# Kernel optimization log

Measured on AMD Instinct MI355X. Metric: run time of the kernel, lower is better.

## Reference

```python
import jax, jax.numpy as jnp
import numpy as np

IN_FEATURES = 512
OUT_FEATURES = 512
N_HEADS = 512
BATCH = 1024
N_REGIONS = 128


def setup_inputs() -> dict:
    key = jax.random.key(0)
    k1, k2, k3, k4 = jax.random.split(key, 4)
    # Match torch's uniform(-stdv, stdv) init scale (stdv = 1/sqrt(last dim))
    stdv_w = 1.0 / np.sqrt(OUT_FEATURES)
    stdv_b = 1.0 / np.sqrt(OUT_FEATURES)
    inputs = {
        "input": jax.random.normal(k1, (IN_FEATURES, BATCH), dtype=jnp.float32),
        "regions_oi": jax.random.randint(k2, (N_REGIONS,), 0, N_HEADS),
        "weight_table": jax.random.uniform(
            k3, (N_HEADS, IN_FEATURES, OUT_FEATURES), dtype=jnp.float32,
            minval=-stdv_w, maxval=stdv_w),
        "bias_table": jax.random.uniform(
            k4, (N_HEADS, OUT_FEATURES), dtype=jnp.float32,
            minval=-stdv_b, maxval=stdv_b),
    }
    return inputs


def reference(input, regions_oi, weight_table, bias_table):
    # Gather per-region weights/biases (EmbeddingTensor lookup)
    w = weight_table[regions_oi]   # (C, A, D) = (n_regions, in_features, out_features)
    b = bias_table[regions_oi]     # (C, D)
    # torch.einsum('ab,cad->cbd', input, w) + b[:, None, :]
    out = jnp.einsum('ab,cad->cbd', input, w) + b[:, None, :]  # (C, B, D)
    return out
```

## Files before the change

kernel.cpp:

```cpp
#include <hip/hip_runtime.h>
#include <stdint.h>

#define A_DIM 512
#define B_DIM 1024
#define D_DIM 512
#define NKT   16

typedef __bf16 bf16x8 __attribute__((ext_vector_type(8)));
typedef float f32x4 __attribute__((ext_vector_type(4)));
typedef unsigned u32x2 __attribute__((ext_vector_type(2)));

typedef __attribute__((address_space(1))) void gvoid_t;
typedef __attribute__((address_space(3))) void svoid_t;

#define WAITV8() asm volatile("s_waitcnt vmcnt(8)" ::: "memory")
#define WAITV0() asm volatile("s_waitcnt vmcnt(0)" ::: "memory")
#define LGKM0()  asm volatile("s_waitcnt lgkmcnt(0)" ::: "memory")
#define FENCE()  asm volatile("" ::: "memory")
#define BARRIER() do { FENCE(); __builtin_amdgcn_s_barrier(); FENCE(); } while (0)

__device__ __forceinline__ unsigned short f2bf(float f) {
  union { float f; unsigned u; } x; x.f = f;
  unsigned r = x.u + 0x7fffu + ((x.u >> 16) & 1u);
  return (unsigned short)(r >> 16);
}

__device__ __forceinline__ unsigned pk2(float lo, float hi) {
  unsigned r;
  asm("v_cvt_pk_bf16_f32 %0, %1, %2" : "=v"(r) : "v"(lo), "v"(hi));
  return r;
}

__device__ __forceinline__ void gload16(const void* g, void* l) {
  __builtin_amdgcn_global_load_lds((gvoid_t*)g, (svoid_t*)l, 16, 0, 0);
}

__global__ __launch_bounds__(256) void transpose_cvt(
    const float* __restrict__ src, unsigned short* __restrict__ dst,
    int M, int N) {
  __shared__ float T[64][65];
  const int t = threadIdx.x;
  const int m0 = blockIdx.y * 64, n0 = blockIdx.x * 64;

#pragma unroll
  for (int p = 0; p < 4; ++p) {
    const int mr = (t >> 4) + p * 16;
    const int n4 = (t & 15) * 4;
    const float4 v = *(const float4*)(src + (size_t)(m0 + mr) * N + n0 + n4);
    T[n4 + 0][mr] = v.x;
    T[n4 + 1][mr] = v.y;
    T[n4 + 2][mr] = v.z;
    T[n4 + 3][mr] = v.w;
  }
  __syncthreads();

#pragma unroll
  for (int p = 0; p < 2; ++p) {
    const int nr = (t >> 3) + p * 32;
    const int m8 = (t & 7) * 8;
    alignas(16) unsigned short tmp[8];
#pragma unroll
    for (int j = 0; j < 8; ++j) tmp[j] = f2bf(T[nr][m8 + j]);
    *(uint4*)(dst + (size_t)(n0 + nr) * M + m0 + m8) = *(const uint4*)tmp;
  }
}

__global__ __launch_bounds__(256, 2) void mlgemm_fused(
    const unsigned short* __restrict__ Xt, const float* __restrict__ wtab,
    const float* __restrict__ bias_table, const int* __restrict__ regions,
    float* __restrict__ out) {
  __shared__ union SM {
    struct {
      alignas(16) unsigned short As[3][256][32];
      alignas(16) unsigned Bsu[2][16][130];
    } k;
    alignas(16) float slab[4][32 * 68];
  } sm;

  const int bid = blockIdx.x;
  const int xcd = bid & 7, q = bid >> 3;
  const int c   = (q >> 4) * 8 + xcd;
  const int t16 = q & 15;
  const int b0     = (t16 & 3) * 256;
  const int d0blk  = (t16 >> 2) * 128;

  const int t = threadIdx.x;
  const int w = t >> 6, l = t & 63;
  const int lr = l & 15, lg = l >> 4;
  const int wm = w >> 1, wn = w & 1;
  const int h = regions[c];

  const unsigned short* Xbase = Xt + (size_t)b0 * A_DIM;
  const float* Wbase = wtab + (size_t)h * A_DIM * D_DIM + d0blk;

  f32x4 acc[8][4] = {};

  const int a_src_chunk = (l & 3) ^ ((l >> 3) & 3);
  const int a_lrow = l >> 2;
  const int kp_base = (w & 1) * 4 + ((l >> 3) & 3);
  const int bd0 = 4 * (l & 7) + 32 * (l >> 5) + 64 * (w >> 1);

  f32x4 bregE[4], bregO[4];

  auto issueA = [&](int T) {
    const int buf = T % 3;
    const int koff = T * 32 + a_src_chunk * 8;
#pragma unroll
    for (int i = 0; i < 4; ++i) {
      const int row0 = w * 64 + i * 16;
      gload16(Xbase + (size_t)(row0 + a_lrow) * A_DIM + koff, &sm.k.As[buf][row0][0]);
    }
  };
  auto ldB = [&](int T, f32x4 (&breg)[4]) {
#pragma unroll
    for (int r = 0; r < 2; ++r) {
      const int kp = r * 8 + kp_base;
      const float* p = Wbase + (size_t)(T * 32 + kp * 2) * D_DIM + bd0;
      breg[r * 2 + 0] = *(const f32x4*)p;
      breg[r * 2 + 1] = *(const f32x4*)(p + D_DIM);
    }
  };
  auto writeB = [&](int T, f32x4 (&breg)[4]) {
#pragma unroll
    for (int r = 0; r < 2; ++r) {
      const int kp = r * 8 + kp_base;
      unsigned pk[4];
#pragma unroll
      for (int i = 0; i < 4; ++i)
        pk[i] = pk2(breg[r * 2][i], breg[r * 2 + 1][i]);
      unsigned* dst = &sm.k.Bsu[T & 1][kp][bd0];
      *(u32x2*)(dst + 0) = u32x2{pk[0], pk[1]};
      *(u32x2*)(dst + 2) = u32x2{pk[2], pk[3]};
    }
  };

  auto mfmaStep = [&](int T) {
    const int abuf = T % 3, bbuf = T & 1;
    bf16x8 av[8], bv[4];
#pragma unroll
    for (int m = 0; m < 8; ++m) {
      const int row = wm * 128 + m * 16 + lr;
      av[m] = *(const bf16x8*)&sm.k.As[abuf][row][(lg ^ ((lr >> 1) & 3)) * 8];
    }
#pragma unroll
    for (int n = 0; n < 4; ++n) {
      const int d = wn * 64 + n * 16 + lr;
      union { unsigned u[4]; bf16x8 v; } ub;
#pragma unroll
      for (int i = 0; i < 4; ++i) ub.u[i] = sm.k.Bsu[bbuf][4 * lg + i][d];
      bv[n] = ub.v;
    }
    __builtin_amdgcn_s_setprio(1);
#pragma unroll
    for (int m = 0; m < 8; ++m)
#pragma unroll
      for (int n = 0; n < 4; ++n)
        acc[m][n] = __builtin_amdgcn_mfma_f32_16x16x32_bf16(av[m], bv[n], acc[m][n], 0, 0, 0);
    __builtin_amdgcn_s_setprio(0);
  };

  float bs[4];
#pragma unroll
  for (int n = 0; n < 4; ++n)
    bs[n] = bias_table[(size_t)h * D_DIM + d0blk + wn * 64 + n * 16 + lr];

  issueA(0); ldB(0, bregE);
  issueA(1); ldB(1, bregO);

#pragma unroll 1
  for (int T = 0; T < NKT - 2; T += 2) {
    WAITV8();
    writeB(T, bregE);
    LGKM0(); BARRIER();
    issueA(T + 2); ldB(T + 2, bregE); FENCE();
    mfmaStep(T);

    WAITV8();
    writeB(T + 1, bregO);
    LGKM0(); BARRIER();
    issueA(T + 3); ldB(T + 3, bregO); FENCE();
    mfmaStep(T + 1);
  }
  WAITV8();
  writeB(NKT - 2, bregE);
  LGKM0(); BARRIER();
  mfmaStep(NKT - 2);
  WAITV0();
  writeB(NKT - 1, bregO);
  LGKM0(); BARRIER();
  mfmaStep(NKT - 1);

  __syncthreads();

  float* ob = out + (size_t)c * B_DIM * D_DIM;
  const int orow_base = b0 + wm * 128;
  const int ocol_base = d0blk + wn * 64;
#pragma unroll
  for (int g = 0; g < 4; ++g) {
#pragma unroll
    for (int m2 = 0; m2 < 2; ++m2)
#pragma unroll
      for (int j = 0; j < 4; ++j) {
        const int row = m2 * 16 + lg * 4 + j;
#pragma unroll
        for (int n = 0; n < 4; ++n)
          sm.slab[w][row * 68 + n * 16 + lr] = acc[g * 2 + m2][n][j] + bs[n];
      }
    __syncthreads();
#pragma unroll
    for (int r = 0; r < 8; ++r) {
      const int chunk = r * 64 + l;
      const int row = chunk >> 4, seg = chunk & 15;
      const f32x4 v = *(const f32x4*)&sm.slab[w][row * 68 + seg * 4];
      __builtin_nontemporal_store(
          v, (f32x4*)(ob + (size_t)(orow_base + g * 32 + row) * D_DIM +
                      ocol_base + seg * 4));
    }
    __syncthreads();
  }
}

__global__ __launch_bounds__(256) void naive_ml(
    const float* __restrict__ in, const int* __restrict__ regions,
    const float* __restrict__ wt, const float* __restrict__ bias,
    float* __restrict__ out) {
  const int d = blockIdx.x * 256 + threadIdx.x;
  const int b = blockIdx.y;
  const int cz = blockIdx.z;
  const int hh = regions[cz];
  const float* W = wt + (size_t)hh * A_DIM * D_DIM + d;
  float acc = bias[(size_t)hh * D_DIM + d];
  for (int a = 0; a < A_DIM; ++a) acc += in[(size_t)a * B_DIM + b] * W[(size_t)a * D_DIM];
  out[(size_t)cz * B_DIM * D_DIM + (size_t)b * D_DIM + d] = acc;
}

extern "C" void kernel_launch(void* const* d_in, const int* in_sizes, int n_in,
                              void* d_out, int out_size, void* d_ws, size_t ws_size,
                              hipStream_t stream) {
  const float* input = (const float*)d_in[0];
  const int* regions = (const int*)d_in[1];
  const float* wtab  = (const float*)d_in[2];
  const float* btab  = (const float*)d_in[3];
  float* out = (float*)d_out;
  const int C = in_sizes[1];

  const size_t xt_bytes = (size_t)B_DIM * A_DIM * 2;

  if (ws_size < xt_bytes) {
    naive_ml<<<dim3(D_DIM / 256, B_DIM, C), 256, 0, stream>>>(input, regions, wtab, btab, out);
    return;
  }

  unsigned short* Xt = (unsigned short*)d_ws;

  transpose_cvt<<<dim3(B_DIM / 64, A_DIM / 64), 256, 0, stream>>>(
      input, Xt, A_DIM, B_DIM);
  mlgemm_fused<<<dim3((B_DIM / 256) * (D_DIM / 128) * C), 256, 0, stream>>>(
      Xt, wtab, btab, regions, out);
}
```

Before: 110.4 us.

## Repack B tile in LDS as k-quad rows for 8-byte fragment reads

Changes how the fp32 weight tile is loaded and staged in LDS. Each wave now loads contiguous 8-byte pairs across the full 128-wide d range for four consecutive k rows, packs them into bf16 quads, and writes one 16-byte store per half. The MFMA B fragment then comes from two 8-byte LDS reads instead of four scalar reads. The vmcnt wait threshold rises to 12 to match the larger number of outstanding global loads per stage. The aim is fewer LDS instructions and cheaper B fragment assembly, at the cost of narrower global loads and possible new bank conflicts.

```diff
diff --git a/kernel.cpp b/kernel.cpp
--- a/kernel.cpp
+++ b/kernel.cpp
@@ -8,15 +8,16 @@
 
 typedef __bf16 bf16x8 __attribute__((ext_vector_type(8)));
 typedef float f32x4 __attribute__((ext_vector_type(4)));
+typedef float f32x2 __attribute__((ext_vector_type(2)));
 typedef unsigned u32x2 __attribute__((ext_vector_type(2)));
 
 typedef __attribute__((address_space(1))) void gvoid_t;
 typedef __attribute__((address_space(3))) void svoid_t;
 
-#define WAITV8() asm volatile("s_waitcnt vmcnt(8)" ::: "memory")
-#define WAITV0() asm volatile("s_waitcnt vmcnt(0)" ::: "memory")
-#define LGKM0()  asm volatile("s_waitcnt lgkmcnt(0)" ::: "memory")
-#define FENCE()  asm volatile("" ::: "memory")
+#define WAITV12() asm volatile("s_waitcnt vmcnt(12)" ::: "memory")
+#define WAITV0()  asm volatile("s_waitcnt vmcnt(0)" ::: "memory")
+#define LGKM0()   asm volatile("s_waitcnt lgkmcnt(0)" ::: "memory")
+#define FENCE()   asm volatile("" ::: "memory")
 #define BARRIER() do { FENCE(); __builtin_amdgcn_s_barrier(); FENCE(); } while (0)
 
 __device__ __forceinline__ unsigned short f2bf(float f) {
@@ -72,7 +73,7 @@
   __shared__ union SM {
     struct {
       alignas(16) unsigned short As[3][256][32];
-      alignas(16) unsigned Bsu[2][16][130];
+      alignas(16) unsigned Bsu[2][8][264];
     } k;
     alignas(16) float slab[4][32 * 68];
   } sm;
@@ -97,10 +98,8 @@
 
   const int a_src_chunk = (l & 3) ^ ((l >> 3) & 3);
   const int a_lrow = l >> 2;
-  const int kp_base = (w & 1) * 4 + ((l >> 3) & 3);
-  const int bd0 = 4 * (l & 7) + 32 * (l >> 5) + 64 * (w >> 1);
-
-  f32x4 bregE[4], bregO[4];
+
+  f32x2 bregE[8], bregO[8];
 
   auto issueA = [&](int T) {
     const int buf = T % 3;
@@ -111,26 +110,28 @@
       gload16(Xbase + (size_t)(row0 + a_lrow) * A_DIM + koff, &sm.k.As[buf][row0][0]);
     }
   };
-  auto ldB = [&](int T, f32x4 (&breg)[4]) {
-#pragma unroll
-    for (int r = 0; r < 2; ++r) {
-      const int kp = r * 8 + kp_base;
-      const float* p = Wbase + (size_t)(T * 32 + kp * 2) * D_DIM + bd0;
-      breg[r * 2 + 0] = *(const f32x4*)p;
-      breg[r * 2 + 1] = *(const f32x4*)(p + D_DIM);
-    }
-  };
-  auto writeB = [&](int T, f32x4 (&breg)[4]) {
-#pragma unroll
-    for (int r = 0; r < 2; ++r) {
-      const int kp = r * 8 + kp_base;
-      unsigned pk[4];
-#pragma unroll
-      for (int i = 0; i < 4; ++i)
-        pk[i] = pk2(breg[r * 2][i], breg[r * 2 + 1][i]);
-      unsigned* dst = &sm.k.Bsu[T & 1][kp][bd0];
-      *(u32x2*)(dst + 0) = u32x2{pk[0], pk[1]};
-      *(u32x2*)(dst + 2) = u32x2{pk[2], pk[3]};
+  auto ldB = [&](int T, f32x2 (&L)[8]) {
+#pragma unroll
+    for (int half = 0; half < 2; ++half) {
+      const int r = w + half * 4;
+#pragma unroll
+      for (int j = 0; j < 4; ++j) {
+        const float* p = Wbase + (size_t)(T * 32 + 4 * r + j) * D_DIM + 2 * l;
+        L[half * 4 + j] = *(const f32x2*)p;
+      }
+    }
+  };
+  auto writeB = [&](int T, f32x2 (&L)[8]) {
+#pragma unroll
+    for (int half = 0; half < 2; ++half) {
+      const int r = w + half * 4;
+      const f32x2* Lq = &L[half * 4];
+      uint4 u;
+      u.x = pk2(Lq[0].x, Lq[1].x);
+      u.y = pk2(Lq[2].x, Lq[3].x);
+      u.z = pk2(Lq[0].y, Lq[1].y);
+      u.w = pk2(Lq[2].y, Lq[3].y);
+      *(uint4*)&sm.k.Bsu[T & 1][r][4 * l] = u;
     }
   };
 
@@ -145,9 +146,9 @@
 #pragma unroll
     for (int n = 0; n < 4; ++n) {
       const int d = wn * 64 + n * 16 + lr;
-      union { unsigned u[4]; bf16x8 v; } ub;
-#pragma unroll
-      for (int i = 0; i < 4; ++i) ub.u[i] = sm.k.Bsu[bbuf][4 * lg + i][d];
+      union { u32x2 p[2]; bf16x8 v; } ub;
+      ub.p[0] = *(const u32x2*)&sm.k.Bsu[bbuf][2 * lg][2 * d];
+      ub.p[1] = *(const u32x2*)&sm.k.Bsu[bbuf][2 * lg + 1][2 * d];
       bv[n] = ub.v;
     }
     __builtin_amdgcn_s_setprio(1);
@@ -169,19 +170,19 @@
 
 #pragma unroll 1
   for (int T = 0; T < NKT - 2; T += 2) {
-    WAITV8();
+    WAITV12();
     writeB(T, bregE);
     LGKM0(); BARRIER();
     issueA(T + 2); ldB(T + 2, bregE); FENCE();
     mfmaStep(T);
 
-    WAITV8();
+    WAITV12();
     writeB(T + 1, bregO);
     LGKM0(); BARRIER();
     issueA(T + 3); ldB(T + 3, bregO); FENCE();
     mfmaStep(T + 1);
   }
-  WAITV8();
+  WAITV12();
   writeB(NKT - 2, bregE);
   LGKM0(); BARRIER();
   mfmaStep(NKT - 2);
```

New measurement: 115.0 us. 1.04x slower.

## Split GEMM tile across 8 waves with smaller per-wave accumulator tiles

Applied to the files above, without the earlier changes.

Doubles the workgroup to 512 threads (8 waves) for the same 256x128 output tile, so each wave now owns a 64x64 subtile instead of 128x64. A/B staging loads and the epilogue slab are redistributed across the extra waves, and the vmcnt wait threshold drops to match the smaller per-thread load count. The aim is more latency hiding and lower register pressure per wave, so more waves fit per CU. The cost is less A-fragment reuse per wave, with more LDS reads per MFMA, and more barrier participants.

```diff
diff --git a/kernel.cpp b/kernel.cpp
--- a/kernel.cpp
+++ b/kernel.cpp
@@ -13,7 +13,7 @@
 typedef __attribute__((address_space(1))) void gvoid_t;
 typedef __attribute__((address_space(3))) void svoid_t;
 
-#define WAITV8() asm volatile("s_waitcnt vmcnt(8)" ::: "memory")
+#define WAITV4() asm volatile("s_waitcnt vmcnt(4)" ::: "memory")
 #define WAITV0() asm volatile("s_waitcnt vmcnt(0)" ::: "memory")
 #define LGKM0()  asm volatile("s_waitcnt lgkmcnt(0)" ::: "memory")
 #define FENCE()  asm volatile("" ::: "memory")
@@ -65,7 +65,7 @@
   }
 }
 
-__global__ __launch_bounds__(256, 2) void mlgemm_fused(
+__global__ __launch_bounds__(512, 4) void mlgemm_fused(
     const unsigned short* __restrict__ Xt, const float* __restrict__ wtab,
     const float* __restrict__ bias_table, const int* __restrict__ regions,
     float* __restrict__ out) {
@@ -74,7 +74,7 @@
       alignas(16) unsigned short As[3][256][32];
       alignas(16) unsigned Bsu[2][16][130];
     } k;
-    alignas(16) float slab[4][32 * 68];
+    alignas(16) float slab[8][16 * 68];
   } sm;
 
   const int bid = blockIdx.x;
@@ -93,53 +93,45 @@
   const unsigned short* Xbase = Xt + (size_t)b0 * A_DIM;
   const float* Wbase = wtab + (size_t)h * A_DIM * D_DIM + d0blk;
 
-  f32x4 acc[8][4] = {};
+  f32x4 acc[4][4] = {};
 
   const int a_src_chunk = (l & 3) ^ ((l >> 3) & 3);
   const int a_lrow = l >> 2;
-  const int kp_base = (w & 1) * 4 + ((l >> 3) & 3);
-  const int bd0 = 4 * (l & 7) + 32 * (l >> 5) + 64 * (w >> 1);
-
-  f32x4 bregE[4], bregO[4];
+  const int kp = w * 2 + (l >> 5);
+  const int bd0 = 4 * (l & 31);
+
+  f32x4 bregE[2], bregO[2];
 
   auto issueA = [&](int T) {
     const int buf = T % 3;
     const int koff = T * 32 + a_src_chunk * 8;
 #pragma unroll
-    for (int i = 0; i < 4; ++i) {
-      const int row0 = w * 64 + i * 16;
+    for (int i = 0; i < 2; ++i) {
+      const int row0 = w * 32 + i * 16;
       gload16(Xbase + (size_t)(row0 + a_lrow) * A_DIM + koff, &sm.k.As[buf][row0][0]);
     }
   };
-  auto ldB = [&](int T, f32x4 (&breg)[4]) {
-#pragma unroll
-    for (int r = 0; r < 2; ++r) {
-      const int kp = r * 8 + kp_base;
-      const float* p = Wbase + (size_t)(T * 32 + kp * 2) * D_DIM + bd0;
-      breg[r * 2 + 0] = *(const f32x4*)p;
-      breg[r * 2 + 1] = *(const f32x4*)(p + D_DIM);
-    }
-  };
-  auto writeB = [&](int T, f32x4 (&breg)[4]) {
-#pragma unroll
-    for (int r = 0; r < 2; ++r) {
-      const int kp = r * 8 + kp_base;
-      unsigned pk[4];
-#pragma unroll
-      for (int i = 0; i < 4; ++i)
-        pk[i] = pk2(breg[r * 2][i], breg[r * 2 + 1][i]);
-      unsigned* dst = &sm.k.Bsu[T & 1][kp][bd0];
-      *(u32x2*)(dst + 0) = u32x2{pk[0], pk[1]};
-      *(u32x2*)(dst + 2) = u32x2{pk[2], pk[3]};
-    }
+  auto ldB = [&](int T, f32x4 (&breg)[2]) {
+    const float* p = Wbase + (size_t)(T * 32 + kp * 2) * D_DIM + bd0;
+    breg[0] = *(const f32x4*)p;
+    breg[1] = *(const f32x4*)(p + D_DIM);
+  };
+  auto writeB = [&](int T, f32x4 (&breg)[2]) {
+    unsigned pk[4];
+#pragma unroll
+    for (int i = 0; i < 4; ++i)
+      pk[i] = pk2(breg[0][i], breg[1][i]);
+    unsigned* dst = &sm.k.Bsu[T & 1][kp][bd0];
+    *(u32x2*)(dst + 0) = u32x2{pk[0], pk[1]};
+    *(u32x2*)(dst + 2) = u32x2{pk[2], pk[3]};
   };
 
   auto mfmaStep = [&](int T) {
     const int abuf = T % 3, bbuf = T & 1;
-    bf16x8 av[8], bv[4];
-#pragma unroll
-    for (int m = 0; m < 8; ++m) {
-      const int row = wm * 128 + m * 16 + lr;
+    bf16x8 av[4], bv[4];
+#pragma unroll
+    for (int m = 0; m < 4; ++m) {
+      const int row = wm * 64 + m * 16 + lr;
       av[m] = *(const bf16x8*)&sm.k.As[abuf][row][(lg ^ ((lr >> 1) & 3)) * 8];
     }
 #pragma unroll
@@ -152,7 +144,7 @@
     }
     __builtin_amdgcn_s_setprio(1);
 #pragma unroll
-    for (int m = 0; m < 8; ++m)
+    for (int m = 0; m < 4; ++m)
 #pragma unroll
       for (int n = 0; n < 4; ++n)
         acc[m][n] = __builtin_amdgcn_mfma_f32_16x16x32_bf16(av[m], bv[n], acc[m][n], 0, 0, 0);
@@ -169,19 +161,19 @@
 
 #pragma unroll 1
   for (int T = 0; T < NKT - 2; T += 2) {
-    WAITV8();
+    WAITV4();
     writeB(T, bregE);
     LGKM0(); BARRIER();
     issueA(T + 2); ldB(T + 2, bregE); FENCE();
     mfmaStep(T);
 
-    WAITV8();
+    WAITV4();
     writeB(T + 1, bregO);
     LGKM0(); BARRIER();
     issueA(T + 3); ldB(T + 3, bregO); FENCE();
     mfmaStep(T + 1);
   }
-  WAITV8();
+  WAITV4();
   writeB(NKT - 2, bregE);
   LGKM0(); BARRIER();
   mfmaStep(NKT - 2);
@@ -193,27 +185,25 @@
   __syncthreads();
 
   float* ob = out + (size_t)c * B_DIM * D_DIM;
-  const int orow_base = b0 + wm * 128;
+  const int orow_base = b0 + wm * 64;
   const int ocol_base = d0blk + wn * 64;
 #pragma unroll
   for (int g = 0; g < 4; ++g) {
 #pragma unroll
-    for (int m2 = 0; m2 < 2; ++m2)
-#pragma unroll
-      for (int j = 0; j < 4; ++j) {
-        const int row = m2 * 16 + lg * 4 + j;
-#pragma unroll
-        for (int n = 0; n < 4; ++n)
-          sm.slab[w][row * 68 + n * 16 + lr] = acc[g * 2 + m2][n][j] + bs[n];
-      }
+    for (int j = 0; j < 4; ++j) {
+      const int row = lg * 4 + j;
+#pragma unroll
+      for (int n = 0; n < 4; ++n)
+        sm.slab[w][row * 68 + n * 16 + lr] = acc[g][n][j] + bs[n];
+    }
     __syncthreads();
 #pragma unroll
-    for (int r = 0; r < 8; ++r) {
+    for (int r = 0; r < 4; ++r) {
       const int chunk = r * 64 + l;
       const int row = chunk >> 4, seg = chunk & 15;
       const f32x4 v = *(const f32x4*)&sm.slab[w][row * 68 + seg * 4];
       __builtin_nontemporal_store(
-          v, (f32x4*)(ob + (size_t)(orow_base + g * 32 + row) * D_DIM +
+          v, (f32x4*)(ob + (size_t)(orow_base + g * 16 + row) * D_DIM +
                       ocol_base + seg * 4));
     }
     __syncthreads();
@@ -255,6 +245,6 @@
 
   transpose_cvt<<<dim3(B_DIM / 64, A_DIM / 64), 256, 0, stream>>>(
       input, Xt, A_DIM, B_DIM);
-  mlgemm_fused<<<dim3((B_DIM / 256) * (D_DIM / 128) * C), 256, 0, stream>>>(
+  mlgemm_fused<<<dim3((B_DIM / 256) * (D_DIM / 128) * C), 512, 0, stream>>>(
       Xt, wtab, btab, regions, out);
 }
```

Result: slower. 162.0 us (+46.7%).
